# Kernel tuning notes

Hardware: AMD Instinct MI355X
Metric: run time of the kernel (lower is better)

The kernel has to match this reference:

```python
import jax, jax.numpy as jnp
import numpy as np

H = 16        # n_heads
D = 1024      # d_model
SPLIT = 4     # number of sequence blocks, each with its own MHA weights
DK = D // H   # head dim
B = 4
SEQ = 4096


def setup_inputs() -> dict:
    key = jax.random.key(0)
    ks = jax.random.split(key, 9)
    sc = 1.0 / np.sqrt(D).astype(np.float32)
    x = jax.random.normal(ks[0], (B, SEQ, D), jnp.float32)
    # Per-split projection weights (torch Linear applied as x @ W + b; random init so
    # the transpose convention is immaterial for a correctness baseline).
    Wq = jax.random.normal(ks[1], (SPLIT, D, D), jnp.float32) * sc
    Wk = jax.random.normal(ks[2], (SPLIT, D, D), jnp.float32) * sc
    Wv = jax.random.normal(ks[3], (SPLIT, D, D), jnp.float32) * sc
    Wo = jax.random.normal(ks[4], (SPLIT, D, D), jnp.float32) * sc
    bq = jax.random.normal(ks[5], (SPLIT, D), jnp.float32) * 0.02
    bk = jax.random.normal(ks[6], (SPLIT, D), jnp.float32) * 0.02
    bv = jax.random.normal(ks[7], (SPLIT, D), jnp.float32) * 0.02
    bo = jax.random.normal(ks[8], (SPLIT, D), jnp.float32) * 0.02
    return {"x": x, "Wq": Wq, "Wk": Wk, "Wv": Wv, "Wo": Wo,
            "bq": bq, "bk": bk, "bv": bv, "bo": bo}


def reference(x, Wq, Wk, Wv, Wo, bq, bk, bv, bo):
    b, l, d = x.shape
    L = l // SPLIT                     # block length
    xs = x.reshape(b, SPLIT, L, d)     # [b, s, L, d] block-diagonal structure

    def proj(W, bias):
        return jnp.einsum('bsld,sde->bsle', xs, W) + bias[None, :, None, :]

    q = proj(Wq, bq).reshape(b, SPLIT, L, H, DK)
    k = proj(Wk, bk).reshape(b, SPLIT, L, H, DK)
    v = proj(Wv, bv).reshape(b, SPLIT, L, H, DK)

    # scaled dot-product attention within each block, causal mask per block
    scores = jnp.einsum('bslhk,bsmhk->bshlm', q, k) / np.sqrt(DK).astype(np.float32)
    causal = jnp.tril(jnp.ones((L, L), dtype=bool))
    scores = jnp.where(causal[None, None, None], scores, jnp.float32(-1e9))
    attn = jax.nn.softmax(scores, axis=-1)   # dropout is identity in eval mode
    o = jnp.einsum('bshlm,bsmhk->bslhk', attn, v).reshape(b, SPLIT, L, d)

    out = jnp.einsum('bsld,sde->bsle', o, Wo) + bo[None, :, None, :]
    return out.reshape(b, l, d)
```

## Files before the change

kernel.cpp:

```cpp
#include <hip/hip_runtime.h>
#include <stdint.h>

#define H_ 16
#define D_ 1024
#define SPLIT_ 4
#define DK_ 64
#define B_ 4
#define SEQ_ 4096
#define L_ 1024

#define QSC 0.18033688f

typedef unsigned short ushort_t;
typedef __attribute__((ext_vector_type(8))) short short8;
typedef __attribute__((ext_vector_type(4))) float floatx4;
typedef __attribute__((ext_vector_type(4))) unsigned short ushortx4;

__device__ __forceinline__ ushort_t f2bf(float f) {
  union { float f; unsigned u; } cv; cv.f = f;
  unsigned u = cv.u;
  return (ushort_t)((u + 0x7fffu + ((u >> 16) & 1u)) >> 16);
}

__device__ __forceinline__ uint32_t pack_bf_trunc(float x, float y) {
#if __has_builtin(__builtin_amdgcn_perm)
  return __builtin_amdgcn_perm(__float_as_uint(y), __float_as_uint(x), 0x07060302u);
#else
  return (__float_as_uint(y) & 0xffff0000u) | (__float_as_uint(x) >> 16);
#endif
}

__device__ __forceinline__ float exp2f_fast(float x) {
#if __has_builtin(__builtin_amdgcn_exp2f)
  return __builtin_amdgcn_exp2f(x);
#else
  return exp2f(x);
#endif
}

__device__ __forceinline__ void gl2lds16(const ushort_t* g, ushort_t* l) {
  __builtin_amdgcn_global_load_lds(
      (const __attribute__((address_space(1))) uint32_t*)g,
      (__attribute__((address_space(3))) uint32_t*)l, 16, 0, 0);
}

__device__ __forceinline__ void wave_barrier() {
  asm volatile("" ::: "memory");
  __builtin_amdgcn_s_barrier();
  asm volatile("" ::: "memory");
}

__global__ __launch_bounds__(256) void convert_x(const float* __restrict__ X,
                                                 ushort_t* __restrict__ Y) {
  const int i = blockIdx.x * 256 + threadIdx.x;
  const float4 v = ((const float4*)X)[i];
  ushortx4 o;
  o[0] = f2bf(v.x); o[1] = f2bf(v.y); o[2] = f2bf(v.z); o[3] = f2bf(v.w);
  ((ushortx4*)Y)[i] = o;
}

__global__ __launch_bounds__(256) void wt_convert_all(const float* __restrict__ W0,
                                                      const float* __restrict__ W1,
                                                      const float* __restrict__ W2,
                                                      const float* __restrict__ W3,
                                                      ushort_t* __restrict__ Wt) {
  __shared__ ushort_t tile[32][33];
  const int z = blockIdx.z, mat = z >> 2, s = z & 3;
  const float* W = (mat == 0) ? W0 : (mat == 1) ? W1 : (mat == 2) ? W2 : W3;
  const float scale = (mat == 0) ? QSC : 1.0f;
  const float* Ws = W + (size_t)s * D_ * D_;
  ushort_t* Wts = Wt + ((size_t)mat * SPLIT_ + s) * D_ * D_;
  const int e0 = blockIdx.x * 32, d0 = blockIdx.y * 32;
  for (int i = threadIdx.y; i < 32; i += 8)
    tile[i][threadIdx.x] = f2bf(Ws[(size_t)(d0 + i) * D_ + e0 + threadIdx.x] * scale);
  __syncthreads();
  for (int i = threadIdx.y; i < 32; i += 8)
    Wts[(size_t)(e0 + i) * D_ + d0 + threadIdx.x] = tile[threadIdx.x][i];
}

__global__ __launch_bounds__(256) void gemm_qkv(const ushort_t* __restrict__ X,
                                                const ushort_t* __restrict__ Wt,
                                                const float* __restrict__ Bq,
                                                const float* __restrict__ Bk,
                                                const float* __restrict__ Bv,
                                                ushort_t* __restrict__ Qo,
                                                ushort_t* __restrict__ Ko,
                                                ushort_t* __restrict__ Vo) {
  __shared__ __attribute__((aligned(16))) ushort_t SH[30720];

  const size_t WT = (size_t)D_ * D_;
  const int xcd = blockIdx.x;
  const int u = blockIdx.y;
  const int bs = xcd + ((u >> 7) << 3);
  const int mn = u & 127;
  const int m0 = (mn & 7) * 128;
  const int n0 = (mn >> 3) * 64;
  const int s = bs & 3;
  const ushort_t* Xb = X + (size_t)bs * (L_ * D_);

  const int t = threadIdx.x;
  const int lane = t & 63;
  const int w = t >> 6;
  const int wm = w >> 1, wn = w & 1;
  const int quad = lane >> 4, cl = lane & 15;
  const int sw = (quad ^ (cl & 3)) * 8;

  floatx4 acc[3][4][2];
  floatx4 zero = {0.f, 0.f, 0.f, 0.f};
#pragma unroll
  for (int mt = 0; mt < 3; ++mt)
#pragma unroll
    for (int i = 0; i < 4; ++i)
#pragma unroll
      for (int j = 0; j < 2; ++j) acc[mt][i][j] = zero;

  const int c0 = t, c1 = t + 256;
  const int r0 = c0 >> 2, cc0 = ((c0 & 3) ^ (r0 & 3)) * 8;
  const int r1 = c1 >> 2, cc1 = ((c1 & 3) ^ (r1 & 3)) * 8;
  const ushort_t* A0 = Xb + (size_t)(m0 + r0) * D_ + cc0;
  const ushort_t* A1 = Xb + (size_t)(m0 + r1) * D_ + cc1;
  const ushort_t* Bsrc0 = Wt + (0 * SPLIT_ + s) * WT + (size_t)(n0 + r0) * D_ + cc0;
  const ushort_t* Bsrc1 = Wt + (1 * SPLIT_ + s) * WT + (size_t)(n0 + r0) * D_ + cc0;
  const ushort_t* Bsrc2 = Wt + (2 * SPLIT_ + s) * WT + (size_t)(n0 + r0) * D_ + cc0;

  auto STAGE = [&](int buf, int k0) {
    gl2lds16(A0 + k0, &SH[buf * 4096 + c0 * 8]);
    gl2lds16(A1 + k0, &SH[buf * 4096 + c1 * 8]);
    gl2lds16(Bsrc0 + k0, &SH[12288 + buf * 6144 + 0 * 2048 + t * 8]);
    gl2lds16(Bsrc1 + k0, &SH[12288 + buf * 6144 + 1 * 2048 + t * 8]);
    gl2lds16(Bsrc2 + k0, &SH[12288 + buf * 6144 + 2 * 2048 + t * 8]);
  };

  auto COMPUTE = [&](int buf) {
    const ushort_t* Ab = &SH[buf * 4096];
    const ushort_t* Bb = &SH[12288 + buf * 6144];
    short8 a[4];
#pragma unroll
    for (int i = 0; i < 4; ++i)
      a[i] = *(const short8*)&Ab[(wm * 64 + i * 16 + cl) * 32 + sw];
#pragma unroll
    for (int mt = 0; mt < 3; ++mt) {
      const ushort_t* Bm = Bb + mt * 2048;
      const short8 b0 = *(const short8*)&Bm[(wn * 32 + cl) * 32 + sw];
      const short8 b1 = *(const short8*)&Bm[(wn * 32 + 16 + cl) * 32 + sw];
#pragma unroll
      for (int i = 0; i < 4; ++i) {
        acc[mt][i][0] = __builtin_amdgcn_mfma_f32_16x16x32_bf16(a[i], b0, acc[mt][i][0], 0, 0, 0);
        acc[mt][i][1] = __builtin_amdgcn_mfma_f32_16x16x32_bf16(a[i], b1, acc[mt][i][1], 0, 0, 0);
      }
    }
  };

  STAGE(0, 0);
  STAGE(1, 32);
#define QKV_STEP(SB, CB, KS)                              \
  STAGE(SB, (KS)*32);                                     \
  asm volatile("s_waitcnt vmcnt(10)" ::: "memory");       \
  wave_barrier();                                         \
  COMPUTE(CB);                                            \
  wave_barrier();
  for (int k3 = 0; k3 < 30; k3 += 3) {
    QKV_STEP(2, 0, k3 + 2)
    QKV_STEP(0, 1, k3 + 3)
    QKV_STEP(1, 2, k3 + 4)
  }
#undef QKV_STEP
  asm volatile("s_waitcnt vmcnt(5)" ::: "memory");
  wave_barrier();
  COMPUTE(0);
  wave_barrier();
  asm volatile("s_waitcnt vmcnt(0)" ::: "memory");
  wave_barrier();
  COMPUTE(1);

  __syncthreads();
  ushort_t* CT = SH;

#pragma unroll
  for (int mt = 0; mt < 2; ++mt) {
    const float* bp = (mt == 0) ? Bq : Bk;
    ushort_t* Og = (mt == 0) ? Qo : Ko;
    const float bscale = (mt == 0) ? QSC : 1.0f;
    float bvj[2];
#pragma unroll
    for (int j = 0; j < 2; ++j)
      bvj[j] = bp[s * D_ + n0 + wn * 32 + j * 16 + cl] * bscale;
#pragma unroll
    for (int i = 0; i < 4; ++i)
#pragma unroll
      for (int j = 0; j < 2; ++j)
#pragma unroll
        for (int r = 0; r < 4; ++r) {
          const int row = wm * 64 + i * 16 + quad * 4 + r;
          const int col = wn * 32 + j * 16 + cl;
          const int ch = col >> 3, off = col & 7;
          CT[row * 64 + ((ch ^ (row & 7)) << 3) + off] = f2bf(acc[mt][i][j][r] + bvj[j]);
        }
    __syncthreads();
#pragma unroll
    for (int pass = 0; pass < 4; ++pass) {
      const int row = pass * 32 + (t >> 3);
      const int ck = t & 7;
      const short8 v = *(const short8*)&CT[row * 64 + ((ck ^ (row & 7)) << 3)];
      *(short8*)(Og + (size_t)bs * (L_ * D_) + (size_t)(m0 + row) * D_ + n0 + ck * 8) = v;
    }
    __syncthreads();
  }

  {
    float bvj[2];
#pragma unroll
    for (int j = 0; j < 2; ++j)
      bvj[j] = Bv[s * D_ + n0 + wn * 32 + j * 16 + cl];
#pragma unroll
    for (int i = 0; i < 4; ++i)
#pragma unroll
      for (int j = 0; j < 2; ++j)
#pragma unroll
        for (int r = 0; r < 4; ++r) {
          const int row = wn * 32 + j * 16 + cl;
          const int col = wm * 64 + i * 16 + quad * 4 + r;
          const int ch = col >> 3, off = col & 7;
          CT[row * 128 + ((ch ^ (row & 15)) << 3) + off] = f2bf(acc[2][i][j][r] + bvj[j]);
        }
    __syncthreads();
#pragma unroll
    for (int pass = 0; pass < 4; ++pass) {
      const int row = pass * 16 + (t >> 4);
      const int ck = t & 15;
      const short8 v = *(const short8*)&CT[row * 128 + ((ck ^ (row & 15)) << 3)];
      *(short8*)(Vo + (size_t)bs * (L_ * D_) + (size_t)(n0 + row) * L_ + m0 + ck * 8) = v;
    }
  }
}

__global__ __launch_bounds__(256) void gemm_o(const ushort_t* __restrict__ X,
                                              const ushort_t* __restrict__ Wt,
                                              const float* __restrict__ bias,
                                              float* __restrict__ C) {
  __shared__ __attribute__((aligned(16))) ushort_t SH[24576];

  const int xcd = blockIdx.x;
  const int u = blockIdx.y;
  const int bs = xcd + ((u >> 6) << 3);
  const int mn = u & 63;
  const int m0 = (mn >> 3) * 128;
  const int n0 = (mn & 7) * 128;
  const int s = bs & 3;
  const ushort_t* Xb = X + (size_t)bs * (L_ * D_);
  const ushort_t* Wts = Wt + (size_t)s * (D_ * D_);

  const int t = threadIdx.x;
  const int lane = t & 63;
  const int w = t >> 6;
  const int wm = w >> 1, wn = w & 1;
  const int quad = lane >> 4, cl = lane & 15;
  const int sw = (quad ^ (cl & 3)) * 8;

  floatx4 acc[4][4];
  floatx4 zero = {0.f, 0.f, 0.f, 0.f};
#pragma unroll
  for (int i = 0; i < 4; ++i)
#pragma unroll
    for (int j = 0; j < 4; ++j) acc[i][j] = zero;

  const int c0 = t, c1 = t + 256;
  const int r0 = c0 >> 2, cc0 = ((c0 & 3) ^ (r0 & 3)) * 8;
  const int r1 = c1 >> 2, cc1 = ((c1 & 3) ^ (r1 & 3)) * 8;
  const ushort_t* A0 = Xb + (size_t)(m0 + r0) * D_ + cc0;
  const ushort_t* A1 = Xb + (size_t)(m0 + r1) * D_ + cc1;
  const ushort_t* B0 = Wts + (size_t)(n0 + r0) * D_ + cc0;
  const ushort_t* B1 = Wts + (size_t)(n0 + r1) * D_ + cc1;

  auto STAGE = [&](int buf, int k0) {
    gl2lds16(A0 + k0, &SH[buf * 4096 + c0 * 8]);
    gl2lds16(A1 + k0, &SH[buf * 4096 + c1 * 8]);
    gl2lds16(B0 + k0, &SH[12288 + buf * 4096 + c0 * 8]);
    gl2lds16(B1 + k0, &SH[12288 + buf * 4096 + c1 * 8]);
  };

  auto COMPUTE = [&](int buf) {
    const ushort_t* As = &SH[buf * 4096];
    const ushort_t* Bs = &SH[12288 + buf * 4096];
    short8 a[4], b[4];
#pragma unroll
    for (int i = 0; i < 4; ++i)
      a[i] = *(const short8*)&As[(wm * 64 + i * 16 + cl) * 32 + sw];
#pragma unroll
    for (int j = 0; j < 4; ++j)
      b[j] = *(const short8*)&Bs[(wn * 64 + j * 16 + cl) * 32 + sw];
#pragma unroll
    for (int i = 0; i < 4; ++i)
#pragma unroll
      for (int j = 0; j < 4; ++j)
        acc[i][j] = __builtin_amdgcn_mfma_f32_16x16x32_bf16(a[i], b[j], acc[i][j], 0, 0, 0);
  };

  STAGE(0, 0);
  STAGE(1, 32);
#define O_STEP(SB, CB, KS)                                \
  STAGE(SB, (KS)*32);                                     \
  asm volatile("s_waitcnt vmcnt(8)" ::: "memory");        \
  wave_barrier();                                         \
  COMPUTE(CB);                                            \
  wave_barrier();
  for (int k3 = 0; k3 < 30; k3 += 3) {
    O_STEP(2, 0, k3 + 2)
    O_STEP(0, 1, k3 + 3)
    O_STEP(1, 2, k3 + 4)
  }
#undef O_STEP
  asm volatile("s_waitcnt vmcnt(4)" ::: "memory");
  wave_barrier();
  COMPUTE(0);
  wave_barrier();
  asm volatile("s_waitcnt vmcnt(0)" ::: "memory");
  wave_barrier();
  COMPUTE(1);

  float bvj[4];
#pragma unroll
  for (int j = 0; j < 4; ++j)
    bvj[j] = bias[s * D_ + n0 + wn * 64 + j * 16 + cl];

#pragma unroll
  for (int j = 0; j < 4; ++j) {
    const int col = n0 + wn * 64 + j * 16 + cl;
#pragma unroll
    for (int i = 0; i < 4; ++i) {
      const int rb = m0 + wm * 64 + i * 16 + quad * 4;
      float* Cf = C + (size_t)bs * (L_ * D_) + (size_t)rb * D_ + col;
#pragma unroll
      for (int r = 0; r < 4; ++r) Cf[(size_t)r * D_] = acc[i][j][r] + bvj[j];
    }
  }
}

__device__ __forceinline__ void attn_step(const ushort_t* __restrict__ Kbuf,
                                          const ushort_t* __restrict__ Vbuf,
                                          ushort_t* __restrict__ PTw,
                                          const short8 qa0, const short8 qa1,
                                          floatx4 (&o)[4], float& m_i, float& l_i,
                                          const bool diag, const int w,
                                          const int quad, const int cl) {
  floatx4 zero = {0.f, 0.f, 0.f, 0.f};
  const int sw0 = (quad ^ (cl & 7)) * 8;
  const int sw1 = ((4 + quad) ^ (cl & 7)) * 8;

  floatx4 st[4];
#pragma unroll
  for (int j = 0; j < 4; ++j) {
    const int row = (j * 16 + cl) * 64;
    const short8 ka0 = *(const short8*)&Kbuf[row + sw0];
    const short8 ka1 = *(const short8*)&Kbuf[row + sw1];
    floatx4 z = zero;
    z = __builtin_amdgcn_mfma_f32_16x16x32_bf16(ka0, qa0, z, 0, 0, 0);
    z = __builtin_amdgcn_mfma_f32_16x16x32_bf16(ka1, qa1, z, 0, 0, 0);
    st[j] = z;
  }

  if (diag) {
    const int ql = w * 16 + cl;
#pragma unroll
    for (int j = 0; j < 4; ++j)
#pragma unroll
      for (int r = 0; r < 4; ++r)
        if (j * 16 + quad * 4 + r > ql) st[j][r] = -1e30f;
  }

  float tm = fmaxf(fmaxf(fmaxf(st[0][0], st[0][1]), fmaxf(st[0][2], st[0][3])),
                   fmaxf(fmaxf(st[1][0], st[1][1]), fmaxf(st[1][2], st[1][3])));
  tm = fmaxf(tm, fmaxf(fmaxf(fmaxf(st[2][0], st[2][1]), fmaxf(st[2][2], st[2][3])),
                       fmaxf(fmaxf(st[3][0], st[3][1]), fmaxf(st[3][2], st[3][3]))));
  tm = fmaxf(tm, __shfl_xor(tm, 16, 64));
  tm = fmaxf(tm, __shfl_xor(tm, 32, 64));
  const float mnew = fmaxf(m_i, tm);
  const float alpha = exp2f_fast(m_i - mnew);
  m_i = mnew;

  float tsv = 0.f;
#pragma unroll
  for (int j = 0; j < 4; ++j)
#pragma unroll
    for (int r = 0; r < 4; ++r) {
      st[j][r] = exp2f_fast(st[j][r] - mnew);
      tsv += st[j][r];
    }
  tsv += __shfl_xor(tsv, 16, 64);
  tsv += __shfl_xor(tsv, 32, 64);
  l_i = l_i * alpha + tsv;

#pragma unroll
  for (int j = 0; j < 4; ++j) {
    const int base = cl * 72 + j * 16 + quad * 4;
    *(uint32_t*)&PTw[base] = pack_bf_trunc(st[j][0], st[j][1]);
    *(uint32_t*)&PTw[base + 2] = pack_bf_trunc(st[j][2], st[j][3]);
  }

#pragma unroll
  for (int j = 0; j < 4; ++j)
#pragma unroll
    for (int r = 0; r < 4; ++r) o[j][r] *= alpha;

  const short8 pb0 = *(const short8*)&PTw[cl * 72 + quad * 8];
  const short8 pb1 = *(const short8*)&PTw[cl * 72 + 32 + quad * 8];
#pragma unroll
  for (int j = 0; j < 4; ++j) {
    const int row = (j * 16 + cl) * 64;
    const short8 va0 = *(const short8*)&Vbuf[row + sw0];
    const short8 va1 = *(const short8*)&Vbuf[row + sw1];
    o[j] = __builtin_amdgcn_mfma_f32_16x16x32_bf16(va0, pb0, o[j], 0, 0, 0);
    o[j] = __builtin_amdgcn_mfma_f32_16x16x32_bf16(va1, pb1, o[j], 0, 0, 0);
  }
}

__device__ __forceinline__ void attn_store(ushort_t* __restrict__ O, size_t act_base,
                                           int qt, int h, const floatx4 (&o)[4],
                                           float l_i, int w, int quad, int cl) {
  const float inv = 1.0f / l_i;
  ushort_t* Orow = O + act_base + (size_t)(qt * 64 + w * 16 + cl) * D_ + h * DK_;
#pragma unroll
  for (int j = 0; j < 4; ++j) {
    ushortx4 pk;
#pragma unroll
    for (int r = 0; r < 4; ++r) pk[r] = f2bf(o[j][r] * inv);
    *(ushortx4*)(Orow + j * 16 + quad * 4) = pk;
  }
}

__global__ __launch_bounds__(256) void attn_kernel(const ushort_t* __restrict__ Q,
                                                   const ushort_t* __restrict__ K,
                                                   const ushort_t* __restrict__ Vt,
                                                   ushort_t* __restrict__ O) {
  __shared__ __attribute__((aligned(16))) ushort_t Ks[2][64 * 64];
  __shared__ __attribute__((aligned(16))) ushort_t Vts[2][64 * 64];
  __shared__ __attribute__((aligned(16))) ushort_t PT[8][1152];

  const int p = blockIdx.x, h = blockIdx.y, bs = blockIdx.z;
  const int t = threadIdx.x, lane = t & 63, w = t >> 6;
  const int quad = lane >> 4, cl = lane & 15;
  const size_t act_base = (size_t)bs * (L_ * D_);
  const int qtA = p, qtB = 15 - p;
  const int NIT = 16 - p;

  const int cA = t, cB = t + 256;
  const int rA = cA >> 3, ccA = ((cA & 7) ^ (rA & 7)) * 8;
  const int rB = cB >> 3, ccB = ((cB & 7) ^ (rB & 7)) * 8;

  const ushort_t* pKA = K + act_base + (size_t)rA * D_ + h * DK_ + ccA;
  const ushort_t* pKB = K + act_base + (size_t)rB * D_ + h * DK_ + ccB;
  const ushort_t* pVA = Vt + act_base + (size_t)(h * DK_ + rA) * L_ + ccA;
  const ushort_t* pVB = Vt + act_base + (size_t)(h * DK_ + rB) * L_ + ccB;
  const size_t kstep = (size_t)64 * D_, vstep = 64;

  floatx4 zero = {0.f, 0.f, 0.f, 0.f};

  const ushort_t* QpA = Q + act_base + (size_t)(qtA * 64 + w * 16 + cl) * D_ + h * DK_ + quad * 8;
  const ushort_t* QpB = Q + act_base + (size_t)(qtB * 64 + w * 16 + cl) * D_ + h * DK_ + quad * 8;
  const short8 qaA0 = *(const short8*)QpA;
  const short8 qaA1 = *(const short8*)(QpA + 32);
  const short8 qaB0 = *(const short8*)QpB;
  const short8 qaB1 = *(const short8*)(QpB + 32);

  floatx4 oA[4], oB[4];
#pragma unroll
  for (int j = 0; j < 4; ++j) { oA[j] = zero; oB[j] = zero; }
  float mA = -3.0e38f, lA = 0.f, mB = -3.0e38f, lB = 0.f;

  gl2lds16(pKA, &Ks[0][cA * 8]);
  gl2lds16(pKB, &Ks[0][cB * 8]);
  gl2lds16(pVA, &Vts[0][cA * 8]);
  gl2lds16(pVB, &Vts[0][cB * 8]);

  for (int kv = 0; kv < NIT; ++kv) {
    __syncthreads();
    if (kv + 1 < NIT) {
      pKA += kstep; pKB += kstep; pVA += vstep; pVB += vstep;
      const int nb = (kv + 1) & 1;
      gl2lds16(pKA, &Ks[nb][cA * 8]);
      gl2lds16(pKB, &Ks[nb][cB * 8]);
      gl2lds16(pVA, &Vts[nb][cA * 8]);
      gl2lds16(pVB, &Vts[nb][cB * 8]);
    }
    const int buf = kv & 1;

    if (kv <= p) {
      attn_step(Ks[buf], Vts[buf], PT[w], qaA0, qaA1, oA, mA, lA,
                kv == p, w, quad, cl);
      if (kv == p) attn_store(O, act_base, qtA, h, oA, lA, w, quad, cl);
    }
    attn_step(Ks[buf], Vts[buf], PT[w + 4], qaB0, qaB1, oB, mB, lB,
              kv == NIT - 1, w, quad, cl);
  }
  attn_store(O, act_base, qtB, h, oB, lB, w, quad, cl);
}

extern "C" void kernel_launch(void* const* d_in, const int* in_sizes, int n_in,
                              void* d_out, int out_size, void* d_ws, size_t ws_size,
                              hipStream_t stream) {
  const float* x  = (const float*)d_in[0];
  const float* Wq = (const float*)d_in[1];
  const float* Wk = (const float*)d_in[2];
  const float* Wv = (const float*)d_in[3];
  const float* Wo = (const float*)d_in[4];
  const float* bq = (const float*)d_in[5];
  const float* bk = (const float*)d_in[6];
  const float* bv = (const float*)d_in[7];
  const float* bo = (const float*)d_in[8];

  const size_t WT_SZ = (size_t)SPLIT_ * D_ * D_;
  const size_t ACT_SZ = (size_t)B_ * SEQ_ * D_;

  ushort_t* ws0 = (ushort_t*)d_ws;
  ushort_t* xbf = ws0;
  ushort_t* wtall = xbf + ACT_SZ;
  ushort_t* wto = wtall + 3 * WT_SZ;
  ushort_t* Vtb = wtall + 4 * WT_SZ;
  ushort_t* Qb = (ushort_t*)d_out;
  ushort_t* Kb = Qb + ACT_SZ;
  ushort_t* Ob = xbf;

  convert_x<<<ACT_SZ / 1024, 256, 0, stream>>>(x, xbf);
  wt_convert_all<<<dim3(32, 32, 16), dim3(32, 8, 1), 0, stream>>>(Wq, Wk, Wv, Wo, wtall);

  gemm_qkv<<<dim3(8, 256, 1), dim3(256, 1, 1), 0, stream>>>(
      xbf, wtall, bq, bk, bv, Qb, Kb, Vtb);

  dim3 ag(8, 16, 16);
  attn_kernel<<<ag, dim3(256, 1, 1), 0, stream>>>(Qb, Kb, Vtb, Ob);

  gemm_o<<<dim3(8, 128, 1), dim3(256, 1, 1), 0, stream>>>(Ob, wto, bo, (float*)d_out);
}
```

Measured before the change: 429.9 us.

## Deepen QKV GEMM pipeline to four LDS buffers, add MFMA priority hints in attention

```diff
diff --git a/kernel.cpp b/kernel.cpp
--- a/kernel.cpp
+++ b/kernel.cpp
@@ -36,6 +36,10 @@
 #else
   return exp2f(x);
 #endif
+}
+
+__device__ __forceinline__ float fmax3(float a, float b, float c) {
+  return fmaxf(fmaxf(a, b), c);
 }
 
 __device__ __forceinline__ void gl2lds16(const ushort_t* g, ushort_t* l) {
@@ -86,7 +90,7 @@
                                                 ushort_t* __restrict__ Qo,
                                                 ushort_t* __restrict__ Ko,
                                                 ushort_t* __restrict__ Vo) {
-  __shared__ __attribute__((aligned(16))) ushort_t SH[30720];
+  __shared__ __attribute__((aligned(16))) ushort_t SH[40960];
 
   const size_t WT = (size_t)D_ * D_;
   const int xcd = blockIdx.x;
@@ -126,14 +130,14 @@
   auto STAGE = [&](int buf, int k0) {
     gl2lds16(A0 + k0, &SH[buf * 4096 + c0 * 8]);
     gl2lds16(A1 + k0, &SH[buf * 4096 + c1 * 8]);
-    gl2lds16(Bsrc0 + k0, &SH[12288 + buf * 6144 + 0 * 2048 + t * 8]);
-    gl2lds16(Bsrc1 + k0, &SH[12288 + buf * 6144 + 1 * 2048 + t * 8]);
-    gl2lds16(Bsrc2 + k0, &SH[12288 + buf * 6144 + 2 * 2048 + t * 8]);
+    gl2lds16(Bsrc0 + k0, &SH[16384 + buf * 6144 + 0 * 2048 + t * 8]);
+    gl2lds16(Bsrc1 + k0, &SH[16384 + buf * 6144 + 1 * 2048 + t * 8]);
+    gl2lds16(Bsrc2 + k0, &SH[16384 + buf * 6144 + 2 * 2048 + t * 8]);
   };
 
   auto COMPUTE = [&](int buf) {
     const ushort_t* Ab = &SH[buf * 4096];
-    const ushort_t* Bb = &SH[12288 + buf * 6144];
+    const ushort_t* Bb = &SH[16384 + buf * 6144];
     short8 a[4];
 #pragma unroll
     for (int i = 0; i < 4; ++i)
@@ -153,25 +157,30 @@
 
   STAGE(0, 0);
   STAGE(1, 32);
-#define QKV_STEP(SB, CB, KS)                              \
-  STAGE(SB, (KS)*32);                                     \
-  asm volatile("s_waitcnt vmcnt(10)" ::: "memory");       \
-  wave_barrier();                                         \
-  COMPUTE(CB);                                            \
-  wave_barrier();
-  for (int k3 = 0; k3 < 30; k3 += 3) {
-    QKV_STEP(2, 0, k3 + 2)
-    QKV_STEP(0, 1, k3 + 3)
-    QKV_STEP(1, 2, k3 + 4)
-  }
-#undef QKV_STEP
-  asm volatile("s_waitcnt vmcnt(5)" ::: "memory");
-  wave_barrier();
-  COMPUTE(0);
+  for (int kb = 0; kb < 7; ++kb) {
+    const int k4 = kb * 128;
+    STAGE(2, k4 + 64);
+    STAGE(3, k4 + 96);
+    asm volatile("s_waitcnt vmcnt(10)" ::: "memory");
+    wave_barrier();
+    COMPUTE(0); COMPUTE(1);
+    wave_barrier();
+    STAGE(0, k4 + 128);
+    STAGE(1, k4 + 160);
+    asm volatile("s_waitcnt vmcnt(10)" ::: "memory");
+    wave_barrier();
+    COMPUTE(2); COMPUTE(3);
+    wave_barrier();
+  }
+  STAGE(2, 960);
+  STAGE(3, 992);
+  asm volatile("s_waitcnt vmcnt(10)" ::: "memory");
+  wave_barrier();
+  COMPUTE(0); COMPUTE(1);
   wave_barrier();
   asm volatile("s_waitcnt vmcnt(0)" ::: "memory");
   wave_barrier();
-  COMPUTE(1);
+  COMPUTE(2); COMPUTE(3);
 
   __syncthreads();
   ushort_t* CT = SH;
@@ -348,6 +357,7 @@
   const int sw1 = ((4 + quad) ^ (cl & 7)) * 8;
 
   floatx4 st[4];
+  __builtin_amdgcn_s_setprio(1);
 #pragma unroll
   for (int j = 0; j < 4; ++j) {
     const int row = (j * 16 + cl) * 64;
@@ -358,6 +368,7 @@
     z = __builtin_amdgcn_mfma_f32_16x16x32_bf16(ka1, qa1, z, 0, 0, 0);
     st[j] = z;
   }
+  __builtin_amdgcn_s_setprio(0);
 
   if (diag) {
     const int ql = w * 16 + cl;
@@ -368,10 +379,12 @@
         if (j * 16 + quad * 4 + r > ql) st[j][r] = -1e30f;
   }
 
-  float tm = fmaxf(fmaxf(fmaxf(st[0][0], st[0][1]), fmaxf(st[0][2], st[0][3])),
-                   fmaxf(fmaxf(st[1][0], st[1][1]), fmaxf(st[1][2], st[1][3])));
-  tm = fmaxf(tm, fmaxf(fmaxf(fmaxf(st[2][0], st[2][1]), fmaxf(st[2][2], st[2][3])),
-                       fmaxf(fmaxf(st[3][0], st[3][1]), fmaxf(st[3][2], st[3][3]))));
+  float t0 = fmax3(st[0][0], st[0][1], st[0][2]);
+  float t1 = fmax3(st[0][3], st[1][0], st[1][1]);
+  float t2 = fmax3(st[1][2], st[1][3], st[2][0]);
+  float t3 = fmax3(st[2][1], st[2][2], st[2][3]);
+  float t4 = fmax3(st[3][0], st[3][1], st[3][2]);
+  float tm = fmaxf(fmax3(t0, t1, t2), fmax3(t3, t4, st[3][3]));
   tm = fmaxf(tm, __shfl_xor(tm, 16, 64));
   tm = fmaxf(tm, __shfl_xor(tm, 32, 64));
   const float mnew = fmaxf(m_i, tm);
@@ -404,6 +417,7 @@
 
   const short8 pb0 = *(const short8*)&PTw[cl * 72 + quad * 8];
   const short8 pb1 = *(const short8*)&PTw[cl * 72 + 32 + quad * 8];
+  __builtin_amdgcn_s_setprio(1);
 #pragma unroll
   for (int j = 0; j < 4; ++j) {
     const int row = (j * 16 + cl) * 64;
@@ -412,6 +426,7 @@
     o[j] = __builtin_amdgcn_mfma_f32_16x16x32_bf16(va0, pb0, o[j], 0, 0, 0);
     o[j] = __builtin_amdgcn_mfma_f32_16x16x32_bf16(va1, pb1, o[j], 0, 0, 0);
   }
+  __builtin_amdgcn_s_setprio(0);
 }
 
 __device__ __forceinline__ void attn_store(ushort_t* __restrict__ O, size_t act_base,
```

New measurement: 460.5 us. 7.1% more time.

## Use MFMA-fragment LDS layout in GEMMs and add setprio around attention MFMAs

Applied to the files above, without the earlier changes.

```diff
diff --git a/kernel.cpp b/kernel.cpp
--- a/kernel.cpp
+++ b/kernel.cpp
@@ -36,6 +36,10 @@
 #else
   return exp2f(x);
 #endif
+}
+
+__device__ __forceinline__ float fmax3(float a, float b, float c) {
+  return fmaxf(fmaxf(a, b), c);
 }
 
 __device__ __forceinline__ void gl2lds16(const ushort_t* g, ushort_t* l) {
@@ -103,7 +107,6 @@
   const int w = t >> 6;
   const int wm = w >> 1, wn = w & 1;
   const int quad = lane >> 4, cl = lane & 15;
-  const int sw = (quad ^ (cl & 3)) * 8;
 
   floatx4 acc[3][4][2];
   floatx4 zero = {0.f, 0.f, 0.f, 0.f};
@@ -114,18 +117,17 @@
 #pragma unroll
       for (int j = 0; j < 2; ++j) acc[mt][i][j] = zero;
 
-  const int c0 = t, c1 = t + 256;
-  const int r0 = c0 >> 2, cc0 = ((c0 & 3) ^ (r0 & 3)) * 8;
-  const int r1 = c1 >> 2, cc1 = ((c1 & 3) ^ (r1 & 3)) * 8;
-  const ushort_t* A0 = Xb + (size_t)(m0 + r0) * D_ + cc0;
-  const ushort_t* A1 = Xb + (size_t)(m0 + r1) * D_ + cc1;
-  const ushort_t* Bsrc0 = Wt + (0 * SPLIT_ + s) * WT + (size_t)(n0 + r0) * D_ + cc0;
-  const ushort_t* Bsrc1 = Wt + (1 * SPLIT_ + s) * WT + (size_t)(n0 + r0) * D_ + cc0;
-  const ushort_t* Bsrc2 = Wt + (2 * SPLIT_ + s) * WT + (size_t)(n0 + r0) * D_ + cc0;
+  const int Ra = ((t >> 6) << 4) + (t & 15);
+  const int ca = ((t >> 4) & 3) * 8;
+  const ushort_t* A0 = Xb + (size_t)(m0 + Ra) * D_ + ca;
+  const ushort_t* A1 = A0 + (size_t)64 * D_;
+  const ushort_t* Bsrc0 = Wt + (0 * SPLIT_ + s) * WT + (size_t)(n0 + Ra) * D_ + ca;
+  const ushort_t* Bsrc1 = Wt + (1 * SPLIT_ + s) * WT + (size_t)(n0 + Ra) * D_ + ca;
+  const ushort_t* Bsrc2 = Wt + (2 * SPLIT_ + s) * WT + (size_t)(n0 + Ra) * D_ + ca;
 
   auto STAGE = [&](int buf, int k0) {
-    gl2lds16(A0 + k0, &SH[buf * 4096 + c0 * 8]);
-    gl2lds16(A1 + k0, &SH[buf * 4096 + c1 * 8]);
+    gl2lds16(A0 + k0, &SH[buf * 4096 + t * 8]);
+    gl2lds16(A1 + k0, &SH[buf * 4096 + (t + 256) * 8]);
     gl2lds16(Bsrc0 + k0, &SH[12288 + buf * 6144 + 0 * 2048 + t * 8]);
     gl2lds16(Bsrc1 + k0, &SH[12288 + buf * 6144 + 1 * 2048 + t * 8]);
     gl2lds16(Bsrc2 + k0, &SH[12288 + buf * 6144 + 2 * 2048 + t * 8]);
@@ -137,12 +139,12 @@
     short8 a[4];
 #pragma unroll
     for (int i = 0; i < 4; ++i)
-      a[i] = *(const short8*)&Ab[(wm * 64 + i * 16 + cl) * 32 + sw];
+      a[i] = *(const short8*)&Ab[(wm * 4 + i) * 512 + lane * 8];
 #pragma unroll
     for (int mt = 0; mt < 3; ++mt) {
       const ushort_t* Bm = Bb + mt * 2048;
-      const short8 b0 = *(const short8*)&Bm[(wn * 32 + cl) * 32 + sw];
-      const short8 b1 = *(const short8*)&Bm[(wn * 32 + 16 + cl) * 32 + sw];
+      const short8 b0 = *(const short8*)&Bm[(wn * 2) * 512 + lane * 8];
+      const short8 b1 = *(const short8*)&Bm[(wn * 2 + 1) * 512 + lane * 8];
 #pragma unroll
       for (int i = 0; i < 4; ++i) {
         acc[mt][i][0] = __builtin_amdgcn_mfma_f32_16x16x32_bf16(a[i], b0, acc[mt][i][0], 0, 0, 0);
@@ -255,7 +257,6 @@
   const int w = t >> 6;
   const int wm = w >> 1, wn = w & 1;
   const int quad = lane >> 4, cl = lane & 15;
-  const int sw = (quad ^ (cl & 3)) * 8;
 
   floatx4 acc[4][4];
   floatx4 zero = {0.f, 0.f, 0.f, 0.f};
@@ -264,19 +265,18 @@
 #pragma unroll
     for (int j = 0; j < 4; ++j) acc[i][j] = zero;
 
-  const int c0 = t, c1 = t + 256;
-  const int r0 = c0 >> 2, cc0 = ((c0 & 3) ^ (r0 & 3)) * 8;
-  const int r1 = c1 >> 2, cc1 = ((c1 & 3) ^ (r1 & 3)) * 8;
-  const ushort_t* A0 = Xb + (size_t)(m0 + r0) * D_ + cc0;
-  const ushort_t* A1 = Xb + (size_t)(m0 + r1) * D_ + cc1;
-  const ushort_t* B0 = Wts + (size_t)(n0 + r0) * D_ + cc0;
-  const ushort_t* B1 = Wts + (size_t)(n0 + r1) * D_ + cc1;
+  const int Ra = ((t >> 6) << 4) + (t & 15);
+  const int ca = ((t >> 4) & 3) * 8;
+  const ushort_t* A0 = Xb + (size_t)(m0 + Ra) * D_ + ca;
+  const ushort_t* A1 = A0 + (size_t)64 * D_;
+  const ushort_t* B0 = Wts + (size_t)(n0 + Ra) * D_ + ca;
+  const ushort_t* B1 = B0 + (size_t)64 * D_;
 
   auto STAGE = [&](int buf, int k0) {
-    gl2lds16(A0 + k0, &SH[buf * 4096 + c0 * 8]);
-    gl2lds16(A1 + k0, &SH[buf * 4096 + c1 * 8]);
-    gl2lds16(B0 + k0, &SH[12288 + buf * 4096 + c0 * 8]);
-    gl2lds16(B1 + k0, &SH[12288 + buf * 4096 + c1 * 8]);
+    gl2lds16(A0 + k0, &SH[buf * 4096 + t * 8]);
+    gl2lds16(A1 + k0, &SH[buf * 4096 + (t + 256) * 8]);
+    gl2lds16(B0 + k0, &SH[12288 + buf * 4096 + t * 8]);
+    gl2lds16(B1 + k0, &SH[12288 + buf * 4096 + (t + 256) * 8]);
   };
 
   auto COMPUTE = [&](int buf) {
@@ -285,10 +285,10 @@
     short8 a[4], b[4];
 #pragma unroll
     for (int i = 0; i < 4; ++i)
-      a[i] = *(const short8*)&As[(wm * 64 + i * 16 + cl) * 32 + sw];
+      a[i] = *(const short8*)&As[(wm * 4 + i) * 512 + lane * 8];
 #pragma unroll
     for (int j = 0; j < 4; ++j)
-      b[j] = *(const short8*)&Bs[(wn * 64 + j * 16 + cl) * 32 + sw];
+      b[j] = *(const short8*)&Bs[(wn * 4 + j) * 512 + lane * 8];
 #pragma unroll
     for (int i = 0; i < 4; ++i)
 #pragma unroll
@@ -348,6 +348,7 @@
   const int sw1 = ((4 + quad) ^ (cl & 7)) * 8;
 
   floatx4 st[4];
+  __builtin_amdgcn_s_setprio(1);
 #pragma unroll
   for (int j = 0; j < 4; ++j) {
     const int row = (j * 16 + cl) * 64;
@@ -358,6 +359,7 @@
     z = __builtin_amdgcn_mfma_f32_16x16x32_bf16(ka1, qa1, z, 0, 0, 0);
     st[j] = z;
   }
+  __builtin_amdgcn_s_setprio(0);
 
   if (diag) {
     const int ql = w * 16 + cl;
@@ -368,10 +370,12 @@
         if (j * 16 + quad * 4 + r > ql) st[j][r] = -1e30f;
   }
 
-  float tm = fmaxf(fmaxf(fmaxf(st[0][0], st[0][1]), fmaxf(st[0][2], st[0][3])),
-                   fmaxf(fmaxf(st[1][0], st[1][1]), fmaxf(st[1][2], st[1][3])));
-  tm = fmaxf(tm, fmaxf(fmaxf(fmaxf(st[2][0], st[2][1]), fmaxf(st[2][2], st[2][3])),
-                       fmaxf(fmaxf(st[3][0], st[3][1]), fmaxf(st[3][2], st[3][3]))));
+  float t0 = fmax3(st[0][0], st[0][1], st[0][2]);
+  float t1 = fmax3(st[0][3], st[1][0], st[1][1]);
+  float t2 = fmax3(st[1][2], st[1][3], st[2][0]);
+  float t3 = fmax3(st[2][1], st[2][2], st[2][3]);
+  float t4 = fmax3(st[3][0], st[3][1], st[3][2]);
+  float tm = fmaxf(fmax3(t0, t1, t2), fmax3(t3, t4, st[3][3]));
   tm = fmaxf(tm, __shfl_xor(tm, 16, 64));
   tm = fmaxf(tm, __shfl_xor(tm, 32, 64));
   const float mnew = fmaxf(m_i, tm);
@@ -404,6 +408,7 @@
 
   const short8 pb0 = *(const short8*)&PTw[cl * 72 + quad * 8];
   const short8 pb1 = *(const short8*)&PTw[cl * 72 + 32 + quad * 8];
+  __builtin_amdgcn_s_setprio(1);
 #pragma unroll
   for (int j = 0; j < 4; ++j) {
     const int row = (j * 16 + cl) * 64;
@@ -412,6 +417,7 @@
     o[j] = __builtin_amdgcn_mfma_f32_16x16x32_bf16(va0, pb0, o[j], 0, 0, 0);
     o[j] = __builtin_amdgcn_mfma_f32_16x16x32_bf16(va1, pb1, o[j], 0, 0, 0);
   }
+  __builtin_amdgcn_s_setprio(0);
 }
 
 __device__ __forceinline__ void attn_store(ushort_t* __restrict__ O, size_t act_base,
```

After: 484.9 us. +12.8%, slower.
